# Kernel optimization log

Hardware: AMD Instinct MI355X
Metric: run time of the kernel (lower is better)

Reference implementation:

```python
import jax, jax.numpy as jnp
import numpy as np

IN_C, OUT_C, MAX_SIZE = 512, 256, 256
N = MAX_SIZE * MAX_SIZE  # 65536 nodes
E = MAX_SIZE * MAX_SIZE  # 65536 edges (before self loops)
NEG_SLOPE = 0.2


def setup_inputs() -> dict:
    key = jax.random.key(0)
    ks = jax.random.split(key, 12)
    s = 1.0 / np.sqrt(IN_C)
    so = 1.0 / np.sqrt(OUT_C)
    return {
        "x": jax.random.normal(ks[0], (N, IN_C), dtype=jnp.float32),
        "x_mask": jnp.ones((N,), dtype=bool),
        "edge_index": jax.random.randint(ks[1], (2, E), 0, N),
        "edge_mask": jnp.ones((E,), dtype=bool),
        "vaild_mask": jnp.ones((MAX_SIZE, MAX_SIZE), dtype=bool),
        # self-loop Linear
        "W_self": jax.random.uniform(ks[2], (IN_C, OUT_C), jnp.float32, -s, s),
        "b_self": jax.random.uniform(ks[3], (OUT_C,), jnp.float32, -s, s),
        # GATv2Conv params (heads=1)
        "W_l": jax.random.uniform(ks[4], (IN_C, OUT_C), jnp.float32, -s, s),
        "b_l": jnp.zeros((OUT_C,), jnp.float32),
        "W_r": jax.random.uniform(ks[5], (IN_C, OUT_C), jnp.float32, -s, s),
        "b_r": jnp.zeros((OUT_C,), jnp.float32),
        "att": jax.random.uniform(ks[6], (OUT_C,), jnp.float32, -so, so),
        "conv_bias": jnp.zeros((OUT_C,), jnp.float32),
        # sk classifier (out_channels -> 1)
        "W_cls": jax.random.uniform(ks[7], (OUT_C, 1), jnp.float32, -so, so),
        "b_cls": jax.random.uniform(ks[8], (1,), jnp.float32, -so, so),
    }


def _forward(x, edge_index, W_self, b_self, W_l, b_l, W_r, b_r, att,
             conv_bias, W_cls, b_cls):
    n = x.shape[0]
    # PyG GATv2Conv adds self-loops by default
    loops = jnp.arange(n, dtype=edge_index.dtype)
    src = jnp.concatenate([edge_index[0], loops])
    dst = jnp.concatenate([edge_index[1], loops])

    x_l = x @ W_l + b_l  # source-side transform (n, out)
    x_r = x @ W_r + b_r  # target-side transform (n, out)

    # per-edge GATv2 attention logits
    h = jax.nn.leaky_relu(x_l[src] + x_r[dst], NEG_SLOPE)  # (Etot, out)
    e = h @ att  # (Etot,)

    # segment softmax over incoming edges of each target node
    m = jnp.full((n,), -jnp.inf, dtype=e.dtype).at[dst].max(e)
    p = jnp.exp(e - m[dst])
    denom = jax.ops.segment_sum(p, dst, num_segments=n)
    alpha = p / denom[dst]

    x_neigh = jax.ops.segment_sum(alpha[:, None] * x_l[src], dst,
                                  num_segments=n) + conv_bias
    x_out = (x @ W_self + b_self) + x_neigh

    # sinkhorn-style row softmax channel (sk_channel=1, n1=n2=max_size)
    ms = MAX_SIZE
    sk = (x_out @ W_cls + b_cls).reshape(ms, ms)
    sk = jax.nn.softmax(sk, axis=-1)
    x_out = x_out + sk.reshape(-1, 1)
    # n1*n2 == max_size**2, so the padded output equals x_out
    return x_out


def reference(x, x_mask, edge_index, edge_mask, vaild_mask, W_self, b_self,
              W_l, b_l, W_r, b_r, att, conv_bias, W_cls, b_cls):
    # masks are all-True (fully valid case): x_valid = x, edges all kept
    return _forward(x, edge_index, W_self, b_self, W_l, b_l, W_r, b_r, att,
                    conv_bias, W_cls, b_cls)
```

## Files before the change

kernel.cpp:

```cpp
#include <hip/hip_runtime.h>
#include <hip/hip_bf16.h>
#include <stdint.h>

#define NNODE 65536
#define NEDGE 65536
#define ETOT  (NNODE + NEDGE)
#define INC   512
#define OUTC  256
#define NEG_SLOPE 0.2f
#define SLOTCAP 32

typedef __attribute__((ext_vector_type(8))) __bf16 bf16x8;
typedef __attribute__((ext_vector_type(4))) float f32x4;

__device__ __forceinline__ float b2f(unsigned short u) {
  return __uint_as_float(((unsigned int)u) << 16);
}
__device__ __forceinline__ unsigned short f2b(float f) {
  unsigned int u = __float_as_uint(f);
  u += 0x7fffu + ((u >> 16) & 1u);
  return (unsigned short)(u >> 16);
}
__device__ __forceinline__ unsigned int pk2(float lo, float hi) {
  return (unsigned int)f2b(lo) | ((unsigned int)f2b(hi) << 16);
}
__device__ __forceinline__ float lrelu(float v) {
  return v > 0.f ? v : NEG_SLOPE * v;
}

__global__ __launch_bounds__(256) void cvt_x_kernel(const float* __restrict__ x,
                                                    unsigned short* __restrict__ xb,
                                                    int* __restrict__ cnt) {
  if (blockIdx.x < 256) cnt[blockIdx.x * 256 + threadIdx.x] = 0;
  size_t i = ((size_t)blockIdx.x * 256 + threadIdx.x) * 8;
  float4 v0 = *(const float4*)(x + i);
  float4 v1 = *(const float4*)(x + i + 4);
  uint4 o;
  o.x = pk2(v0.x, v0.y);
  o.y = pk2(v0.z, v0.w);
  o.z = pk2(v1.x, v1.y);
  o.w = pk2(v1.z, v1.w);
  *(uint4*)(xb + i) = o;
}

__global__ __launch_bounds__(256) void prep_w_kernel(
    const float* __restrict__ Wl, const float* __restrict__ Wr, const float* __restrict__ Ws,
    const float* __restrict__ bl, const float* __restrict__ br, const float* __restrict__ bs,
    unsigned short* __restrict__ WT, float* __restrict__ bcat) {
  int i = blockIdx.x * 256 + threadIdx.x;
  if (i < 768 * 512) {
    int o = i >> 9, k = i & 511;
    float v;
    if (o < 256)      v = Wl[k * 256 + o];
    else if (o < 512) v = Wr[k * 256 + (o - 256)];
    else              v = Ws[k * 256 + (o - 512)];
    WT[i] = f2b(v);
  }
  if (i < 768) {
    bcat[i] = (i < 256) ? bl[i] : (i < 512 ? br[i - 256] : bs[i - 512]);
  }
}

__global__ __launch_bounds__(512) void gemm_kernel(
    const unsigned short* __restrict__ Xb,
    const unsigned short* __restrict__ WT,
    const float* __restrict__ bcat,
    unsigned short* __restrict__ xl,
    unsigned short* __restrict__ xr,
    unsigned short* __restrict__ xs) {
  __shared__ __align__(16) char smem[98304];
  unsigned short* ring = (unsigned short*)smem;

  const int wid = blockIdx.x;
  const int xcd = wid & 7;
  const int local = wid >> 3;
  const int by = local % 3;
  const int rowt = xcd * 32 + local / 3;
  const int rowBase = rowt * 256;
  const int colBase = by * 256;

  const int tid = threadIdx.x;
  const int lane = tid & 63;
  const int w = tid >> 6;
  const int wm = (w >> 2) * 128;
  const int wn = (w & 3) * 64;

  f32x4 acc[8][4] = {};

  auto stageh = [&](int c, int hf) {
    const int kk = c * 32;
    const int buf = c % 3;
    const int q = tid;
    const int sl = q & 3;
    const unsigned short* basep = hf ? (WT + (size_t)colBase * 512) : (Xb + (size_t)rowBase * 512);
    unsigned short* ldst = ring + buf * 16384 + hf * 8192;
#pragma unroll
    for (int l = 0; l < 2; ++l) {
      const int r = l * 128 + (q >> 2);
      const int slot = sl ^ ((r >> 1) & 3);
      const unsigned short* g = basep + (size_t)r * 512 + kk + slot * 8;
      __builtin_amdgcn_global_load_lds(
          (const __attribute__((address_space(1))) void*)g,
          (__attribute__((address_space(3))) void*)(ldst + l * 4096 + q * 8), 16, 0, 0);
    }
  };

  stageh(0, 0); stageh(0, 1);
  stageh(1, 0); stageh(1, 1);
  asm volatile("s_waitcnt vmcnt(4)" ::: "memory");
  __builtin_amdgcn_s_barrier();

#pragma unroll
  for (int c = 0; c < 16; ++c) {
    const unsigned short* As = ring + (c % 3) * 16384;
    const unsigned short* Bs = As + 8192;
    const int kq = lane >> 4;
    bf16x8 fa[8], fb[4];

#pragma unroll
    for (int m = 0; m < 4; ++m) {
      const int rA = wm + m * 16 + (lane & 15);
      fa[m] = *(const bf16x8*)&As[rA * 32 + ((kq ^ ((rA >> 1) & 3)) << 3)];
    }
#pragma unroll
    for (int n = 0; n < 4; ++n) {
      const int rB = wn + n * 16 + (lane & 15);
      fb[n] = *(const bf16x8*)&Bs[rB * 32 + ((kq ^ ((rB >> 1) & 3)) << 3)];
    }
    if (c + 2 < 16) stageh(c + 2, 0);
    __builtin_amdgcn_s_barrier();
    asm volatile("s_waitcnt lgkmcnt(0)" ::: "memory");
    __builtin_amdgcn_sched_barrier(0);
    __builtin_amdgcn_s_setprio(1);
#pragma unroll
    for (int m = 0; m < 4; ++m)
#pragma unroll
      for (int n = 0; n < 4; ++n)
        acc[m][n] = __builtin_amdgcn_mfma_f32_16x16x32_bf16(fa[m], fb[n], acc[m][n], 0, 0, 0);
    __builtin_amdgcn_s_setprio(0);
    __builtin_amdgcn_s_barrier();

#pragma unroll
    for (int m = 4; m < 8; ++m) {
      const int rA = wm + m * 16 + (lane & 15);
      fa[m] = *(const bf16x8*)&As[rA * 32 + ((kq ^ ((rA >> 1) & 3)) << 3)];
    }
    if (c + 2 < 16) stageh(c + 2, 1);
    __builtin_amdgcn_s_barrier();
    asm volatile("s_waitcnt lgkmcnt(0)" ::: "memory");
    __builtin_amdgcn_sched_barrier(0);
    __builtin_amdgcn_s_setprio(1);
#pragma unroll
    for (int m = 4; m < 8; ++m)
#pragma unroll
      for (int n = 0; n < 4; ++n)
        acc[m][n] = __builtin_amdgcn_mfma_f32_16x16x32_bf16(fa[m], fb[n], acc[m][n], 0, 0, 0);
    __builtin_amdgcn_s_setprio(0);
    if (c <= 13)      asm volatile("s_waitcnt vmcnt(4)" ::: "memory");
    else if (c == 14) asm volatile("s_waitcnt vmcnt(0)" ::: "memory");
    __builtin_amdgcn_s_barrier();
  }

  {
    unsigned short* dst = (by == 0) ? xl : (by == 1) ? xr : xs;
    float* eps = (float*)smem + w * 1088;
    float biasn[4];
#pragma unroll
    for (int n = 0; n < 4; ++n) biasn[n] = bcat[colBase + wn + n * 16 + (lane & 15)];
#pragma unroll
    for (int m = 0; m < 8; ++m) {
#pragma unroll
      for (int n = 0; n < 4; ++n)
#pragma unroll
        for (int j = 0; j < 4; ++j)
          eps[((lane >> 4) * 4 + j) * 68 + n * 16 + (lane & 15)] = acc[m][n][j] + biasn[n];
#pragma unroll
      for (int it = 0; it < 2; ++it) {
        const int r16 = it * 8 + (lane >> 3);
        const int c8 = (lane & 7) * 8;
        const float* srcp = eps + r16 * 68 + c8;
        float4 v0 = *(const float4*)srcp;
        float4 v1 = *(const float4*)(srcp + 4);
        uint4 o;
        o.x = pk2(v0.x, v0.y);
        o.y = pk2(v0.z, v0.w);
        o.z = pk2(v1.x, v1.y);
        o.w = pk2(v1.z, v1.w);
        *(uint4*)(dst + (size_t)(rowBase + wm + m * 16 + r16) * 256 + wn + c8) = o;
      }
    }
  }
}

__global__ __launch_bounds__(256) void edge_logit_kernel(
    const int* __restrict__ ei,
    const unsigned short* __restrict__ xl,
    const unsigned short* __restrict__ xr,
    const float* __restrict__ att,
    int* __restrict__ cnt,
    int* __restrict__ slot_src,
    float* __restrict__ slot_e) {
  const int j = blockIdx.x * 8 + (threadIdx.x >> 5);
  const int lane = threadIdx.x & 31;
  int src, dst;
  if (j < NEDGE) { src = ei[j]; dst = ei[NEDGE + j]; }
  else           { src = j - NEDGE; dst = src; }
  const int c = lane * 8;
  uint4 ul = *(const uint4*)(xl + (size_t)src * 256 + c);
  uint4 ur = *(const uint4*)(xr + (size_t)dst * 256 + c);
  float4 a0 = *(const float4*)(att + c);
  float4 a1 = *(const float4*)(att + c + 4);
  float s = lrelu(b2f((unsigned short)ul.x) + b2f((unsigned short)ur.x)) * a0.x
          + lrelu(b2f((unsigned short)(ul.x >> 16)) + b2f((unsigned short)(ur.x >> 16))) * a0.y
          + lrelu(b2f((unsigned short)ul.y) + b2f((unsigned short)ur.y)) * a0.z
          + lrelu(b2f((unsigned short)(ul.y >> 16)) + b2f((unsigned short)(ur.y >> 16))) * a0.w
          + lrelu(b2f((unsigned short)ul.z) + b2f((unsigned short)ur.z)) * a1.x
          + lrelu(b2f((unsigned short)(ul.z >> 16)) + b2f((unsigned short)(ur.z >> 16))) * a1.y
          + lrelu(b2f((unsigned short)ul.w) + b2f((unsigned short)ur.w)) * a1.z
          + lrelu(b2f((unsigned short)(ul.w >> 16)) + b2f((unsigned short)(ur.w >> 16))) * a1.w;
#pragma unroll
  for (int off = 16; off; off >>= 1) s += __shfl_xor(s, off);
  if (lane == 0) {
    const int pos = atomicAdd(&cnt[dst], 1);
    if (pos < SLOTCAP) {
      slot_src[dst * SLOTCAP + pos] = src;
      slot_e[dst * SLOTCAP + pos] = s;
    }
  }
}

__global__ __launch_bounds__(256) void node_kernel(
    const int* __restrict__ cnt,
    const int* __restrict__ slot_src, const float* __restrict__ slot_e,
    const unsigned short* __restrict__ xl,
    const unsigned short* __restrict__ xs,
    const float* __restrict__ conv_bias,
    float* __restrict__ out,
    const float* __restrict__ Wcls, const float* __restrict__ bcls,
    float* __restrict__ logits) {
  const int n = blockIdx.x * 4 + (threadIdx.x >> 6);
  const int lane = threadIdx.x & 63;
  const int base = n * SLOTCAP;
  const int deg = cnt[n];

  float m = -1e30f;
  for (int k = 0; k < deg; ++k) m = fmaxf(m, slot_e[base + k]);
  float denom = 0.f;
  for (int k = 0; k < deg; ++k) denom += __expf(slot_e[base + k] - m);
  const float inv = 1.f / denom;

  const int c = lane * 4;
  float4 accv = {0.f, 0.f, 0.f, 0.f};
  for (int k = 0; k < deg; ++k) {
    const float alpha = __expf(slot_e[base + k] - m) * inv;
    const int src = slot_src[base + k];
    ushort4 u = *(const ushort4*)(xl + (size_t)src * 256 + c);
    accv.x += alpha * b2f(u.x);
    accv.y += alpha * b2f(u.y);
    accv.z += alpha * b2f(u.z);
    accv.w += alpha * b2f(u.w);
  }
  ushort4 s4 = *(const ushort4*)(xs + (size_t)n * 256 + c);
  float4 cb = *(const float4*)(conv_bias + c);
  float4 cur;
  cur.x = b2f(s4.x) + accv.x + cb.x;
  cur.y = b2f(s4.y) + accv.y + cb.y;
  cur.z = b2f(s4.z) + accv.z + cb.z;
  cur.w = b2f(s4.w) + accv.w + cb.w;
  const size_t o = (size_t)n * 256 + c;
  *(float4*)(out + o) = cur;

  float4 wc = *(const float4*)(Wcls + c);
  float part = cur.x * wc.x + cur.y * wc.y + cur.z * wc.z + cur.w * wc.w;
#pragma unroll
  for (int off = 32; off; off >>= 1) part += __shfl_xor(part, off, 64);
  if (lane == 0) logits[n] = part + bcls[0];
}

__global__ __launch_bounds__(256) void sk_kernel(const float* __restrict__ logits,
                                                 float* __restrict__ out) {
  __shared__ float sv[256];
  __shared__ float red[256];
  const int r = blockIdx.x >> 2;
  const int q = blockIdx.x & 3;
  const int t = threadIdx.x;
  const float v = logits[r * 256 + t];
  red[t] = v;
  __syncthreads();
  for (int d = 128; d; d >>= 1) {
    if (t < d) red[t] = fmaxf(red[t], red[t + d]);
    __syncthreads();
  }
  const float mx = red[0];
  __syncthreads();
  const float p = __expf(v - mx);
  red[t] = p;
  __syncthreads();
  for (int d = 128; d; d >>= 1) {
    if (t < d) red[t] += red[t + d];
    __syncthreads();
  }
  const float sum = red[0];
  sv[t] = p / sum;
  __syncthreads();
  const size_t rowbase = (size_t)r * 256 * 256;
  for (int i = q * 64; i < q * 64 + 64; ++i) {
    out[rowbase + (size_t)i * 256 + t] += sv[i];
  }
}

extern "C" void kernel_launch(void* const* d_in, const int* in_sizes, int n_in,
                              void* d_out, int out_size, void* d_ws, size_t ws_size,
                              hipStream_t stream) {
  const float* x        = (const float*)d_in[0];
  const int*   ei       = (const int*)d_in[2];
  const float* W_self   = (const float*)d_in[5];
  const float* b_self   = (const float*)d_in[6];
  const float* W_l      = (const float*)d_in[7];
  const float* b_l      = (const float*)d_in[8];
  const float* W_r      = (const float*)d_in[9];
  const float* b_r      = (const float*)d_in[10];
  const float* att      = (const float*)d_in[11];
  const float* conv_bias= (const float*)d_in[12];
  const float* W_cls    = (const float*)d_in[13];
  const float* b_cls    = (const float*)d_in[14];
  float* out = (float*)d_out;

  char* ws = (char*)d_ws;
  size_t off = 0;
  auto alloc = [&](size_t bytes) {
    char* p = ws + off;
    off += (bytes + 255) & ~(size_t)255;
    return p;
  };
  unsigned short* xb   = (unsigned short*)alloc((size_t)NNODE * INC * 2);
  unsigned short* WT   = (unsigned short*)alloc((size_t)768 * 512 * 2);
  float*          bcat = (float*)alloc(768 * 4);
  unsigned short* xlb  = (unsigned short*)alloc((size_t)NNODE * OUTC * 2);
  unsigned short* xrb  = (unsigned short*)alloc((size_t)NNODE * OUTC * 2);
  unsigned short* xsb  = (unsigned short*)alloc((size_t)NNODE * OUTC * 2);
  int*            cnt  = (int*)alloc((size_t)NNODE * 4);
  float*          logits  = (float*)alloc((size_t)NNODE * 4);
  int*   slot_src = (int*)xb;
  float* slot_e   = (float*)(xb + (size_t)NNODE * SLOTCAP * 2);
  (void)ws_size; (void)in_sizes; (void)n_in; (void)out_size;

  cvt_x_kernel<<<(NNODE * INC) / (256 * 8), 256, 0, stream>>>(x, xb, cnt);
  prep_w_kernel<<<(768 * 512 + 255) / 256, 256, 0, stream>>>(W_l, W_r, W_self, b_l, b_r, b_self, WT, bcat);
  gemm_kernel<<<768, 512, 0, stream>>>(xb, WT, bcat, xlb, xrb, xsb);
  edge_logit_kernel<<<ETOT / 8, 256, 0, stream>>>(ei, xlb, xrb, att, cnt, slot_src, slot_e);
  node_kernel<<<NNODE / 4, 256, 0, stream>>>(cnt, slot_src, slot_e, xlb, xsb, conv_bias,
                                             out, W_cls, b_cls, logits);
  sk_kernel<<<1024, 256, 0, stream>>>(logits, out);
}
```

Before: 199.8 us.

## Precompute classifier logits via linearity and fuse row softmax into node kernel

Computes per-node projections of xl and xs onto W_cls in the GEMM epilogue. A lightweight per-node kernel then forms the classifier logits from the attention weights, before the main aggregation. The row softmax is then applied inside the node kernel, so the output is written once instead of being re-read and updated by a separate sk kernel. Bias terms constant per row are dropped because softmax is shift-invariant. This adds epilogue shuffles and one extra small kernel pass over the slot arrays.

```diff
diff --git a/kernel.cpp b/kernel.cpp
--- a/kernel.cpp
+++ b/kernel.cpp
@@ -65,9 +65,12 @@
     const unsigned short* __restrict__ Xb,
     const unsigned short* __restrict__ WT,
     const float* __restrict__ bcat,
+    const float* __restrict__ Wcls,
     unsigned short* __restrict__ xl,
     unsigned short* __restrict__ xr,
-    unsigned short* __restrict__ xs) {
+    unsigned short* __restrict__ xs,
+    float* __restrict__ g,
+    float* __restrict__ gs) {
   __shared__ __align__(16) char smem[98304];
   unsigned short* ring = (unsigned short*)smem;
 
@@ -98,9 +101,9 @@
     for (int l = 0; l < 2; ++l) {
       const int r = l * 128 + (q >> 2);
       const int slot = sl ^ ((r >> 1) & 3);
-      const unsigned short* g = basep + (size_t)r * 512 + kk + slot * 8;
+      const unsigned short* gp = basep + (size_t)r * 512 + kk + slot * 8;
       __builtin_amdgcn_global_load_lds(
-          (const __attribute__((address_space(1))) void*)g,
+          (const __attribute__((address_space(1))) void*)gp,
           (__attribute__((address_space(3))) void*)(ldst + l * 4096 + q * 8), 16, 0, 0);
     }
   };
@@ -163,17 +166,26 @@
 
   {
     unsigned short* dst = (by == 0) ? xl : (by == 1) ? xr : xs;
+    const bool doG = (by != 1);
     float* eps = (float*)smem + w * 1088;
-    float biasn[4];
-#pragma unroll
-    for (int n = 0; n < 4; ++n) biasn[n] = bcat[colBase + wn + n * 16 + (lane & 15)];
+    float* gpart = (float*)(smem + 40960);
+    float biasn[4], wcn[4];
+#pragma unroll
+    for (int n = 0; n < 4; ++n) {
+      biasn[n] = bcat[colBase + wn + n * 16 + (lane & 15)];
+      wcn[n] = Wcls[wn + n * 16 + (lane & 15)];
+    }
 #pragma unroll
     for (int m = 0; m < 8; ++m) {
+      float rp[4] = {0.f, 0.f, 0.f, 0.f};
 #pragma unroll
       for (int n = 0; n < 4; ++n)
 #pragma unroll
-        for (int j = 0; j < 4; ++j)
-          eps[((lane >> 4) * 4 + j) * 68 + n * 16 + (lane & 15)] = acc[m][n][j] + biasn[n];
+        for (int j = 0; j < 4; ++j) {
+          const float v = acc[m][n][j] + biasn[n];
+          eps[((lane >> 4) * 4 + j) * 68 + n * 16 + (lane & 15)] = v;
+          rp[j] += v * wcn[n];
+        }
 #pragma unroll
       for (int it = 0; it < 2; ++it) {
         const int r16 = it * 8 + (lane >> 3);
@@ -188,6 +200,23 @@
         o.w = pk2(v1.z, v1.w);
         *(uint4*)(dst + (size_t)(rowBase + wm + m * 16 + r16) * 256 + wn + c8) = o;
       }
+      if (doG) {
+#pragma unroll
+        for (int j = 0; j < 4; ++j) {
+          float s = rp[j];
+          s += __shfl_xor(s, 1);
+          s += __shfl_xor(s, 2);
+          s += __shfl_xor(s, 4);
+          s += __shfl_xor(s, 8);
+          if ((lane & 15) == 0)
+            gpart[(wm + m * 16 + (lane >> 4) * 4 + j) * 4 + (w & 3)] = s;
+        }
+      }
+    }
+    __syncthreads();
+    if (doG && tid < 256) {
+      float s = gpart[tid * 4] + gpart[tid * 4 + 1] + gpart[tid * 4 + 2] + gpart[tid * 4 + 3];
+      ((by == 0) ? g : gs)[rowBase + tid] = s;
     }
   }
 }
@@ -229,15 +258,33 @@
   }
 }
 
-__global__ __launch_bounds__(256) void node_kernel(
+__global__ __launch_bounds__(256) void logit_kernel(
+    const int* __restrict__ cnt,
+    const int* __restrict__ slot_src, const float* __restrict__ slot_e,
+    const float* __restrict__ g, const float* __restrict__ gs,
+    float* __restrict__ logits) {
+  const int n = blockIdx.x * 256 + threadIdx.x;
+  const int base = n * SLOTCAP;
+  const int deg = cnt[n];
+  float m = -1e30f;
+  for (int k = 0; k < deg; ++k) m = fmaxf(m, slot_e[base + k]);
+  float denom = 0.f, wsum = 0.f;
+  for (int k = 0; k < deg; ++k) {
+    const float p = __expf(slot_e[base + k] - m);
+    denom += p;
+    wsum += p * g[slot_src[base + k]];
+  }
+  logits[n] = gs[n] + wsum / denom;
+}
+
+__global__ __launch_bounds__(256) void node_sk_kernel(
     const int* __restrict__ cnt,
     const int* __restrict__ slot_src, const float* __restrict__ slot_e,
     const unsigned short* __restrict__ xl,
     const unsigned short* __restrict__ xs,
     const float* __restrict__ conv_bias,
-    float* __restrict__ out,
-    const float* __restrict__ Wcls, const float* __restrict__ bcls,
-    float* __restrict__ logits) {
+    const float* __restrict__ logits,
+    float* __restrict__ out) {
   const int n = blockIdx.x * 4 + (threadIdx.x >> 6);
   const int lane = threadIdx.x & 63;
   const int base = n * SLOTCAP;
@@ -260,53 +307,25 @@
     accv.z += alpha * b2f(u.z);
     accv.w += alpha * b2f(u.w);
   }
+
+  const int r = n >> 8;
+  float4 lv = *(const float4*)(logits + r * 256 + c);
+  float lm = fmaxf(fmaxf(lv.x, lv.y), fmaxf(lv.z, lv.w));
+#pragma unroll
+  for (int off = 32; off; off >>= 1) lm = fmaxf(lm, __shfl_xor(lm, off));
+  float ls = __expf(lv.x - lm) + __expf(lv.y - lm) + __expf(lv.z - lm) + __expf(lv.w - lm);
+#pragma unroll
+  for (int off = 32; off; off >>= 1) ls += __shfl_xor(ls, off);
+  const float softval = __expf(logits[n] - lm) / ls;
+
   ushort4 s4 = *(const ushort4*)(xs + (size_t)n * 256 + c);
   float4 cb = *(const float4*)(conv_bias + c);
   float4 cur;
-  cur.x = b2f(s4.x) + accv.x + cb.x;
-  cur.y = b2f(s4.y) + accv.y + cb.y;
-  cur.z = b2f(s4.z) + accv.z + cb.z;
-  cur.w = b2f(s4.w) + accv.w + cb.w;
-  const size_t o = (size_t)n * 256 + c;
-  *(float4*)(out + o) = cur;
-
-  float4 wc = *(const float4*)(Wcls + c);
-  float part = cur.x * wc.x + cur.y * wc.y + cur.z * wc.z + cur.w * wc.w;
-#pragma unroll
-  for (int off = 32; off; off >>= 1) part += __shfl_xor(part, off, 64);
-  if (lane == 0) logits[n] = part + bcls[0];
-}
-
-__global__ __launch_bounds__(256) void sk_kernel(const float* __restrict__ logits,
-                                                 float* __restrict__ out) {
-  __shared__ float sv[256];
-  __shared__ float red[256];
-  const int r = blockIdx.x >> 2;
-  const int q = blockIdx.x & 3;
-  const int t = threadIdx.x;
-  const float v = logits[r * 256 + t];
-  red[t] = v;
-  __syncthreads();
-  for (int d = 128; d; d >>= 1) {
-    if (t < d) red[t] = fmaxf(red[t], red[t + d]);
-    __syncthreads();
-  }
-  const float mx = red[0];
-  __syncthreads();
-  const float p = __expf(v - mx);
-  red[t] = p;
-  __syncthreads();
-  for (int d = 128; d; d >>= 1) {
-    if (t < d) red[t] += red[t + d];
-    __syncthreads();
-  }
-  const float sum = red[0];
-  sv[t] = p / sum;
-  __syncthreads();
-  const size_t rowbase = (size_t)r * 256 * 256;
-  for (int i = q * 64; i < q * 64 + 64; ++i) {
-    out[rowbase + (size_t)i * 256 + t] += sv[i];
-  }
+  cur.x = b2f(s4.x) + accv.x + cb.x + softval;
+  cur.y = b2f(s4.y) + accv.y + cb.y + softval;
+  cur.z = b2f(s4.z) + accv.z + cb.z + softval;
+  cur.w = b2f(s4.w) + accv.w + cb.w + softval;
+  *(float4*)(out + (size_t)n * 256 + c) = cur;
 }
 
 extern "C" void kernel_launch(void* const* d_in, const int* in_sizes, int n_in,
@@ -323,7 +342,6 @@
   const float* att      = (const float*)d_in[11];
   const float* conv_bias= (const float*)d_in[12];
   const float* W_cls    = (const float*)d_in[13];
-  const float* b_cls    = (const float*)d_in[14];
   float* out = (float*)d_out;
 
   char* ws = (char*)d_ws;
@@ -341,15 +359,17 @@
   unsigned short* xsb  = (unsigned short*)alloc((size_t)NNODE * OUTC * 2);
   int*            cnt  = (int*)alloc((size_t)NNODE * 4);
   float*          logits  = (float*)alloc((size_t)NNODE * 4);
+  float*          gbuf    = (float*)alloc((size_t)NNODE * 4);
+  float*          gsbuf   = (float*)alloc((size_t)NNODE * 4);
   int*   slot_src = (int*)xb;
   float* slot_e   = (float*)(xb + (size_t)NNODE * SLOTCAP * 2);
   (void)ws_size; (void)in_sizes; (void)n_in; (void)out_size;
 
   cvt_x_kernel<<<(NNODE * INC) / (256 * 8), 256, 0, stream>>>(x, xb, cnt);
   prep_w_kernel<<<(768 * 512 + 255) / 256, 256, 0, stream>>>(W_l, W_r, W_self, b_l, b_r, b_self, WT, bcat);
-  gemm_kernel<<<768, 512, 0, stream>>>(xb, WT, bcat, xlb, xrb, xsb);
+  gemm_kernel<<<768, 512, 0, stream>>>(xb, WT, bcat, W_cls, xlb, xrb, xsb, gbuf, gsbuf);
   edge_logit_kernel<<<ETOT / 8, 256, 0, stream>>>(ei, xlb, xrb, att, cnt, slot_src, slot_e);
-  node_kernel<<<NNODE / 4, 256, 0, stream>>>(cnt, slot_src, slot_e, xlb, xsb, conv_bias,
-                                             out, W_cls, b_cls, logits);
-  sk_kernel<<<1024, 256, 0, stream>>>(logits, out);
-}
+  logit_kernel<<<NNODE / 256, 256, 0, stream>>>(cnt, slot_src, slot_e, gbuf, gsbuf, logits);
+  node_sk_kernel<<<NNODE / 4, 256, 0, stream>>>(cnt, slot_src, slot_e, xlb, xsb, conv_bias,
+                                                logits, out);
+}
```

Result: faster. 191.0 us (median of 2 runs) (-4.4%).
